# Kernel optimization log

Hardware: AMD Instinct MI355X
Metric: run time of the kernel (lower is better)

Reference implementation:

```python
import jax, jax.numpy as jnp
import numpy as np

N = 100000   # n_nodes (= ninput, identity features)
E = 1600000  # edges per adjacency (avg degree 16)
H = 128      # nhid
EPS = 1e-12


def setup_inputs() -> dict:
    key = jax.random.key(0)
    ks = jax.random.split(key, 24)
    inp = {
        'adj1_rows': jax.random.randint(ks[0], (E,), 0, N),
        'adj1_cols': jax.random.randint(ks[1], (E,), 0, N),
        'adj1_vals': jax.random.uniform(ks[2], (E,), jnp.float32) / 16.0,
        'adj2_rows': jax.random.randint(ks[3], (E,), 0, N),
        'adj2_cols': jax.random.randint(ks[4], (E,), 0, N),
        'adj2_vals': jax.random.uniform(ks[5], (E,), jnp.float32) / 16.0,
    }
    s = 1.0 / np.sqrt(H)
    inp['w1'] = jax.random.uniform(ks[6], (N, H), jnp.float32, -s, s)
    for i in range(2, 10):
        inp[f'w{i}'] = jax.random.uniform(ks[5 + i], (H, H), jnp.float32, -s, s)
    s2 = 1.0 / np.sqrt(2 * H)
    inp['m1'] = jax.random.uniform(ks[15], (H, 2 * H), jnp.float32, -s, s)
    inp['b1'] = jnp.zeros((2 * H,), jnp.float32)
    inp['m2'] = jax.random.uniform(ks[16], (2 * H, 2 * H), jnp.float32, -s2, s2)
    inp['b2'] = jnp.zeros((2 * H,), jnp.float32)
    inp['m3'] = jax.random.uniform(ks[17], (2 * H, 1), jnp.float32, -s2, s2)
    inp['b3'] = jnp.zeros((1,), jnp.float32)
    return inp


def _spmm(rows, cols, vals, x):
    # sparse [N,N] @ dense [N,H] via gather + segment_sum
    return jax.ops.segment_sum(vals[:, None] * x[cols], rows, num_segments=N)


def _l2norm(x):
    # F.normalize(x, p=2, dim=1)
    n = jnp.sqrt(jnp.sum(x * x, axis=1, keepdims=True))
    return x / jnp.maximum(n, EPS)


def _mlp(x, m1, b1, m2, b2, m3, b3):
    # dropout inactive (eval mode) for deterministic reference
    h = jax.nn.relu(x @ m1 + b1)
    h = jax.nn.relu(h @ m2 + b2)
    return h @ m3 + b3  # [N,1]


def _branch(rows, cols, vals, w1, ws, mlp_params):
    x = jax.nn.relu(_spmm(rows, cols, vals, w1))
    x = _l2norm(x)
    score = _mlp(x, *mlp_params)
    for i, w in enumerate(ws):
        x = jax.nn.relu(_spmm(rows, cols, vals, x @ w))
        if i < len(ws) - 1:  # last layer (gc9) is relu only, no normalize
            x = _l2norm(x)
        score = score + _mlp(x, *mlp_params)
    return score


def reference(adj1_rows, adj1_cols, adj1_vals, adj2_rows, adj2_cols, adj2_vals,
              w1, w2, w3, w4, w5, w6, w7, w8, w9,
              m1, b1, m2, b2, m3, b3):
    ws = [w2, w3, w4, w5, w6, w7, w8, w9]
    mlp_params = (m1, b1, m2, b2, m3, b3)
    score1 = _branch(adj1_rows, adj1_cols, adj1_vals, w1, ws, mlp_params)
    score2 = _branch(adj2_rows, adj2_cols, adj2_vals, w1, ws, mlp_params)
    return score1 * score2  # [N,1]
```

## Files before the change

kernel.cpp:

```cpp
#include <hip/hip_runtime.h>
#include <hip/hip_fp16.h>

#define NN 100000
#define NE 1600000
#define HD 128
#define HD2 256

typedef unsigned int u32;
typedef unsigned short u16;
typedef _Float16 half8 __attribute__((ext_vector_type(8)));
typedef float floatx4 __attribute__((ext_vector_type(4)));

static inline int cdiv(int a, int b){ return (a + b - 1) / b; }

__device__ __forceinline__ u32 split_pack(float v){
  __half h;
  if(fabsf(v) < 6.103515625e-05f) h = __ushort_as_half((u16)0);
  else h = __float2half_rn(v);
  float hf = __half2float(h);
  __half l = __float2half_rn((v - hf) * 4096.0f);
  return (u32)__half_as_ushort(h) | ((u32)__half_as_ushort(l) << 16);
}

__global__ void k_zero_int(int* __restrict__ p, int n){
  int i = blockIdx.x * 256 + threadIdx.x;
  if(i < n) p[i] = 0;
}

__global__ void k_zero_f2(float* __restrict__ a, float* __restrict__ b, int n){
  int i = blockIdx.x * 256 + threadIdx.x;
  if(i < n){ a[i] = 0.f; b[i] = 0.f; }
}

__global__ void k_hist(const int* __restrict__ rows, int* __restrict__ cnt){
  int e = blockIdx.x * 256 + threadIdx.x;
  if(e < NE) atomicAdd(&cnt[rows[e]], 1);
}

__global__ void k_scan1(const int* __restrict__ cnt, int* __restrict__ part,
                        int* __restrict__ sums, int n){
  __shared__ int sh[256];
  int tid = threadIdx.x;
  int base = blockIdx.x * 1024 + tid * 4;
  int v0 = (base + 0 < n) ? cnt[base + 0] : 0;
  int v1 = (base + 1 < n) ? cnt[base + 1] : 0;
  int v2 = (base + 2 < n) ? cnt[base + 2] : 0;
  int v3 = (base + 3 < n) ? cnt[base + 3] : 0;
  int s = v0 + v1 + v2 + v3;
  sh[tid] = s;
  __syncthreads();
  for(int d = 1; d < 256; d <<= 1){
    int t = (tid >= d) ? sh[tid - d] : 0;
    __syncthreads();
    sh[tid] += t;
    __syncthreads();
  }
  int excl = sh[tid] - s;
  if(tid == 255) sums[blockIdx.x] = sh[255];
  if(base + 0 < n) part[base + 0] = excl;
  if(base + 1 < n) part[base + 1] = excl + v0;
  if(base + 2 < n) part[base + 2] = excl + v0 + v1;
  if(base + 3 < n) part[base + 3] = excl + v0 + v1 + v2;
}

__global__ void k_scan2(int* __restrict__ sums, int nb){
  __shared__ int sh[128];
  int tid = threadIdx.x;
  int v = (tid < nb) ? sums[tid] : 0;
  sh[tid] = v;
  __syncthreads();
  for(int d = 1; d < 128; d <<= 1){
    int t = (tid >= d) ? sh[tid - d] : 0;
    __syncthreads();
    sh[tid] += t;
    __syncthreads();
  }
  if(tid < nb) sums[tid] = sh[tid] - v;
}

__global__ void k_scan3(int* __restrict__ rowptr, int* __restrict__ cursor,
                        const int* __restrict__ sums, int n){
  int tid = threadIdx.x;
  int off = sums[blockIdx.x];
  int base = blockIdx.x * 1024 + tid * 4;
  #pragma unroll
  for(int j = 0; j < 4; j++){
    int idx = base + j;
    if(idx < n){ int r = rowptr[idx] + off; rowptr[idx] = r; cursor[idx] = r; }
  }
  if(blockIdx.x == 0 && tid == 0) rowptr[n] = NE;
}

__global__ void k_scatter(const int* __restrict__ rows, const int* __restrict__ cols,
                          const float* __restrict__ vals, int* __restrict__ cursor,
                          int* __restrict__ ocol, float* __restrict__ oval){
  int e = blockIdx.x * 256 + threadIdx.x;
  if(e < NE){
    int r = rows[e];
    int pp = atomicAdd(&cursor[r], 1);
    ocol[pp] = cols[e];
    oval[pp] = vals[e];
  }
}

__global__ void k_splitw(const float* __restrict__ W, u32* __restrict__ out,
                         int K, int N, int total){
  int idx = blockIdx.x * 256 + threadIdx.x;
  if(idx < total){
    int n = idx / K, k = idx - n * K;
    out[idx] = split_pack(W[(size_t)k * N + n]);
  }
}

template<bool NORM>
__global__ void k_spmm(const int* __restrict__ rowptr, const int* __restrict__ col,
                       const float* __restrict__ val, const float* __restrict__ X,
                       u32* __restrict__ outpk){
  int node = (blockIdx.x << 2) + (threadIdx.x >> 6);
  int lane = threadIdx.x & 63;
  if(node >= NN) return;
  int s = rowptr[node], e = rowptr[node + 1];
  float ax = 0.f, ay = 0.f, bx = 0.f, by = 0.f;
  float cx = 0.f, cy = 0.f, dx = 0.f, dy = 0.f;
  int i = s;
  for(; i + 7 < e; i += 8){
    int   c0 = col[i],     c1 = col[i + 1], c2 = col[i + 2], c3 = col[i + 3];
    int   c4 = col[i + 4], c5 = col[i + 5], c6 = col[i + 6], c7 = col[i + 7];
    float v0 = val[i],     v1 = val[i + 1], v2 = val[i + 2], v3 = val[i + 3];
    float v4 = val[i + 4], v5 = val[i + 5], v6 = val[i + 6], v7 = val[i + 7];
    float2 x0 = *(const float2*)(X + (size_t)c0 * HD + lane * 2);
    float2 x1 = *(const float2*)(X + (size_t)c1 * HD + lane * 2);
    float2 x2 = *(const float2*)(X + (size_t)c2 * HD + lane * 2);
    float2 x3 = *(const float2*)(X + (size_t)c3 * HD + lane * 2);
    float2 x4 = *(const float2*)(X + (size_t)c4 * HD + lane * 2);
    float2 x5 = *(const float2*)(X + (size_t)c5 * HD + lane * 2);
    float2 x6 = *(const float2*)(X + (size_t)c6 * HD + lane * 2);
    float2 x7 = *(const float2*)(X + (size_t)c7 * HD + lane * 2);
    ax += v0 * x0.x + v1 * x1.x;  ay += v0 * x0.y + v1 * x1.y;
    bx += v2 * x2.x + v3 * x3.x;  by += v2 * x2.y + v3 * x3.y;
    cx += v4 * x4.x + v5 * x5.x;  cy += v4 * x4.y + v5 * x5.y;
    dx += v6 * x6.x + v7 * x7.x;  dy += v6 * x6.y + v7 * x7.y;
  }
  for(; i + 1 < e; i += 2){
    int   c0 = col[i],   c1 = col[i + 1];
    float v0 = val[i],   v1 = val[i + 1];
    float2 x0 = *(const float2*)(X + (size_t)c0 * HD + lane * 2);
    float2 x1 = *(const float2*)(X + (size_t)c1 * HD + lane * 2);
    ax += v0 * x0.x + v1 * x1.x;  ay += v0 * x0.y + v1 * x1.y;
  }
  if(i < e){
    int c = col[i]; float v = val[i];
    float2 xv = *(const float2*)(X + (size_t)c * HD + lane * 2);
    ax += v * xv.x; ay += v * xv.y;
  }
  ax += bx + cx + dx;
  ay += by + cy + dy;
  ax = fmaxf(ax, 0.f);
  ay = fmaxf(ay, 0.f);
  if(NORM){
    float ss = ax * ax + ay * ay;
    #pragma unroll
    for(int o = 32; o >= 1; o >>= 1) ss += __shfl_xor(ss, o, 64);
    float scale = 1.f / fmaxf(sqrtf(ss), 1e-12f);
    ax *= scale; ay *= scale;
  }
  *(uint2*)(outpk + (size_t)node * HD + lane * 2) = make_uint2(split_pack(ax), split_pack(ay));
}

template<int MODE>
__launch_bounds__(256, 2)
__global__ void k_mfma_gemm(const u32* __restrict__ Apk, const u32* __restrict__ Btpk,
                            const float* __restrict__ bias, float* __restrict__ Yout,
                            u32* __restrict__ Hout, const float* __restrict__ m3,
                            float* __restrict__ score, int M, int K, int N){
  __shared__ unsigned short As_h[128 * 40], As_l[128 * 40];
  __shared__ unsigned short Bs_h[128 * 40], Bs_l[128 * 40];
  const int tid = threadIdx.x;
  const int lane = tid & 63, wid = tid >> 6;
  const int lm = lane & 15, lg = lane >> 4;
  const int mq = (wid & 1) * 64, nq = (wid >> 1) * 64;
  const int m0 = blockIdx.x * 128, n0 = blockIdx.y * 128;

  floatx4 accA[4][4], accB[4][4];
  #pragma unroll
  for(int i = 0; i < 4; i++)
    #pragma unroll
    for(int j = 0; j < 4; j++){
      accA[i][j] = (floatx4){0.f, 0.f, 0.f, 0.f};
      accB[i][j] = (floatx4){0.f, 0.f, 0.f, 0.f};
    }

  for(int k0 = 0; k0 < K; k0 += 32){
    uint4 av[4], bv[4];
    #pragma unroll
    for(int j = 0; j < 4; j++){
      int li = tid + j * 256;
      int row = li >> 3, kc = (li & 7) * 4;
      int ar = m0 + row; if(ar >= M) ar = M - 1;
      av[j] = *(const uint4*)(Apk + (size_t)ar * K + k0 + kc);
      bv[j] = *(const uint4*)(Btpk + (size_t)(n0 + row) * K + k0 + kc);
    }
    __syncthreads();
    #pragma unroll
    for(int j = 0; j < 4; j++){
      int li = tid + j * 256;
      int row = li >> 3, kc = (li & 7) * 4;
      int base = row * 40 + kc;
      ushort4 h, l;
      h.x = (u16)(av[j].x & 0xffff); l.x = (u16)(av[j].x >> 16);
      h.y = (u16)(av[j].y & 0xffff); l.y = (u16)(av[j].y >> 16);
      h.z = (u16)(av[j].z & 0xffff); l.z = (u16)(av[j].z >> 16);
      h.w = (u16)(av[j].w & 0xffff); l.w = (u16)(av[j].w >> 16);
      *(ushort4*)&As_h[base] = h;
      *(ushort4*)&As_l[base] = l;
      h.x = (u16)(bv[j].x & 0xffff); l.x = (u16)(bv[j].x >> 16);
      h.y = (u16)(bv[j].y & 0xffff); l.y = (u16)(bv[j].y >> 16);
      h.z = (u16)(bv[j].z & 0xffff); l.z = (u16)(bv[j].z >> 16);
      h.w = (u16)(bv[j].w & 0xffff); l.w = (u16)(bv[j].w >> 16);
      *(ushort4*)&Bs_h[base] = h;
      *(ushort4*)&Bs_l[base] = l;
    }
    __syncthreads();

    half8 fa_h[4], fa_l[4], fb_h[4], fb_l[4];
    #pragma unroll
    for(int s = 0; s < 4; s++){
      int ra = (mq + s * 16 + lm) * 40 + lg * 8;
      fa_h[s] = *(const half8*)&As_h[ra];
      fa_l[s] = *(const half8*)&As_l[ra];
      int rb = (nq + s * 16 + lm) * 40 + lg * 8;
      fb_h[s] = *(const half8*)&Bs_h[rb];
      fb_l[s] = *(const half8*)&Bs_l[rb];
    }
    #pragma unroll
    for(int i = 0; i < 4; i++)
      #pragma unroll
      for(int j = 0; j < 4; j++){
        accA[i][j] = __builtin_amdgcn_mfma_f32_16x16x32_f16(fa_h[i], fb_h[j], accA[i][j], 0, 0, 0);
        accB[i][j] = __builtin_amdgcn_mfma_f32_16x16x32_f16(fa_h[i], fb_l[j], accB[i][j], 0, 0, 0);
        accB[i][j] = __builtin_amdgcn_mfma_f32_16x16x32_f16(fa_l[i], fb_h[j], accB[i][j], 0, 0, 0);
      }
  }

  const float inv4096 = 1.f / 4096.f;
  if(MODE == 0){
    #pragma unroll
    for(int i = 0; i < 4; i++)
      #pragma unroll
      for(int r = 0; r < 4; r++){
        int m = m0 + mq + i * 16 + lg * 4 + r;
        if(m < M){
          #pragma unroll
          for(int j = 0; j < 4; j++){
            int c = n0 + nq + j * 16 + lm;
            Yout[(size_t)m * N + c] = accA[i][j][r] + accB[i][j][r] * inv4096;
          }
        }
      }
  } else if(MODE == 1){
    #pragma unroll
    for(int i = 0; i < 4; i++)
      #pragma unroll
      for(int r = 0; r < 4; r++){
        int m = m0 + mq + i * 16 + lg * 4 + r;
        if(m < M){
          #pragma unroll
          for(int j = 0; j < 4; j++){
            int c = n0 + nq + j * 16 + lm;
            float v = fmaxf(accA[i][j][r] + accB[i][j][r] * inv4096 + bias[c], 0.f);
            Hout[(size_t)m * N + c] = split_pack(v);
          }
        }
      }
  } else {
    #pragma unroll
    for(int i = 0; i < 4; i++)
      #pragma unroll
      for(int r = 0; r < 4; r++){
        float s = 0.f;
        #pragma unroll
        for(int j = 0; j < 4; j++){
          int c = n0 + nq + j * 16 + lm;
          float v = fmaxf(accA[i][j][r] + accB[i][j][r] * inv4096 + bias[c], 0.f);
          s = fmaf(v, m3[c], s);
        }
        s += __shfl_xor(s, 1, 64);
        s += __shfl_xor(s, 2, 64);
        s += __shfl_xor(s, 4, 64);
        s += __shfl_xor(s, 8, 64);
        int m = m0 + mq + i * 16 + lg * 4 + r;
        if(lm == 0 && m < M) atomicAdd(&score[m], s);
      }
  }
}

__global__ void k_final(const float* __restrict__ s1, const float* __restrict__ s2,
                        const float* __restrict__ b3, float* __restrict__ out){
  int i = blockIdx.x * 256 + threadIdx.x;
  if(i < NN){
    float b = 9.f * b3[0];
    out[i] = (s1[i] + b) * (s2[i] + b);
  }
}

extern "C" void kernel_launch(void* const* d_in, const int* in_sizes, int n_in,
                              void* d_out, int out_size, void* d_ws, size_t ws_size,
                              hipStream_t stream){
  const int*   a1r = (const int*)d_in[0];
  const int*   a1c = (const int*)d_in[1];
  const float* a1v = (const float*)d_in[2];
  const int*   a2r = (const int*)d_in[3];
  const int*   a2c = (const int*)d_in[4];
  const float* a2v = (const float*)d_in[5];
  const float* w1  = (const float*)d_in[6];
  const float* w[8];
  for(int i = 0; i < 8; i++) w[i] = (const float*)d_in[7 + i];
  const float* m1 = (const float*)d_in[15];
  const float* b1 = (const float*)d_in[16];
  const float* m2 = (const float*)d_in[17];
  const float* b2 = (const float*)d_in[18];
  const float* m3 = (const float*)d_in[19];
  const float* b3 = (const float*)d_in[20];
  float* out = (float*)d_out;

  char* base = (char*)d_ws;
  size_t off = 0;
  auto alloc = [&](size_t bytes) -> char* {
    char* r = base + off;
    off += (bytes + 255) & ~(size_t)255;
    return r;
  };
  int*   c1ptr = (int*)  alloc((size_t)(NN + 1) * 4);
  int*   c1col = (int*)  alloc((size_t)NE * 4);
  float* c1val = (float*)alloc((size_t)NE * 4);
  int*   c2ptr = (int*)  alloc((size_t)(NN + 1) * 4);
  int*   c2col = (int*)  alloc((size_t)NE * 4);
  float* c2val = (float*)alloc((size_t)NE * 4);
  int*   cursor= (int*)  alloc((size_t)NN * 4);
  int*   sums  = (int*)  alloc(512);
  u32*   xpk   = (u32*)  alloc((size_t)NN * HD * 4);
  u32*   h1pk  = (u32*)  alloc((size_t)NN * HD2 * 4);
  float* sc1   = (float*)alloc((size_t)NN * 4);
  float* sc2   = (float*)alloc((size_t)NN * 4);
  u32*   wtpk[8];
  for(int i = 0; i < 8; i++) wtpk[i] = (u32*)alloc((size_t)HD * HD * 4);
  u32*   m1tpk = (u32*)alloc((size_t)HD2 * HD * 4);
  u32*   m2tpk = (u32*)alloc((size_t)HD2 * HD2 * 4);
  float* y = (float*)h1pk;

  const int SCAN_BLOCKS = cdiv(NN, 1024);
  auto build_csr = [&](const int* rows, const int* cols, const float* vals,
                       int* rptr, int* rcol, float* rval){
    hipLaunchKernelGGL(k_zero_int, dim3(cdiv(NN, 256)), dim3(256), 0, stream, cursor, NN);
    hipLaunchKernelGGL(k_hist,     dim3(cdiv(NE, 256)), dim3(256), 0, stream, rows, cursor);
    hipLaunchKernelGGL(k_scan1,    dim3(SCAN_BLOCKS),   dim3(256), 0, stream, cursor, rptr, sums, NN);
    hipLaunchKernelGGL(k_scan2,    dim3(1),             dim3(128), 0, stream, sums, SCAN_BLOCKS);
    hipLaunchKernelGGL(k_scan3,    dim3(SCAN_BLOCKS),   dim3(256), 0, stream, rptr, cursor, sums, NN);
    hipLaunchKernelGGL(k_scatter,  dim3(cdiv(NE, 256)), dim3(256), 0, stream, rows, cols, vals, cursor, rcol, rval);
  };

  auto splitw = [&](const float* W, u32* o, int K, int N){
    int total = K * N;
    hipLaunchKernelGGL(k_splitw, dim3(cdiv(total, 256)), dim3(256), 0, stream, W, o, K, N, total);
  };
  for(int i = 0; i < 8; i++) splitw(w[i], wtpk[i], HD, HD);
  splitw(m1, m1tpk, HD, HD2);
  splitw(m2, m2tpk, HD2, HD2);

  const int GX = cdiv(NN, 128);
  auto mlp = [&](float* score){
    hipLaunchKernelGGL((k_mfma_gemm<1>), dim3(GX, 2), dim3(256), 0, stream,
                       xpk, m1tpk, b1, (float*)nullptr, h1pk,
                       (const float*)nullptr, (float*)nullptr, NN, HD, HD2);
    hipLaunchKernelGGL((k_mfma_gemm<2>), dim3(GX, 2), dim3(256), 0, stream,
                       h1pk, m2tpk, b2, (float*)nullptr, (u32*)nullptr,
                       m3, score, NN, HD2, HD2);
  };

  auto branch = [&](const int* rptr, const int* rcol, const float* rval, float* score){
    hipLaunchKernelGGL((k_spmm<true>), dim3(cdiv(NN, 4)), dim3(256), 0, stream,
                       rptr, rcol, rval, w1, xpk);
    mlp(score);
    for(int i = 0; i < 8; i++){
      hipLaunchKernelGGL((k_mfma_gemm<0>), dim3(GX, 1), dim3(256), 0, stream,
                         xpk, wtpk[i], (const float*)nullptr, y, (u32*)nullptr,
                         (const float*)nullptr, (float*)nullptr, NN, HD, HD);
      if(i < 7)
        hipLaunchKernelGGL((k_spmm<true>),  dim3(cdiv(NN, 4)), dim3(256), 0, stream,
                           rptr, rcol, rval, y, xpk);
      else
        hipLaunchKernelGGL((k_spmm<false>), dim3(cdiv(NN, 4)), dim3(256), 0, stream,
                           rptr, rcol, rval, y, xpk);
      mlp(score);
    }
  };

  build_csr(a1r, a1c, a1v, c1ptr, c1col, c1val);
  build_csr(a2r, a2c, a2v, c2ptr, c2col, c2val);
  hipLaunchKernelGGL(k_zero_f2, dim3(cdiv(NN, 256)), dim3(256), 0, stream, sc1, sc2, NN);
  branch(c1ptr, c1col, c1val, sc1);
  branch(c2ptr, c2col, c2val, sc2);
  hipLaunchKernelGGL(k_final, dim3(cdiv(NN, 256)), dim3(256), 0, stream, sc1, sc2, b3, out);
}
```

Baseline: 4.860 ms.

## Batch both graph branches into single launches and widen SpMM unroll

Runs the two adjacency branches together: CSR construction, SpMM (via a z grid dimension), and the GEMM/MLP launches now cover 2*N rows when workspace allows, with a fallback to the per-branch path. This halves kernel launch count and gives each GEMM and SpMM launch more blocks to fill the GPU. The SpMM inner loop is also unrolled to 16 gathers in flight. The cost is double-sized intermediate buffers and higher register use in the SpMM kernel.

Result: no change. 4.847 ms (-0.3%).

```diff
diff --git a/kernel.cpp b/kernel.cpp
--- a/kernel.cpp
+++ b/kernel.cpp
@@ -27,25 +27,33 @@
   if(i < n) p[i] = 0;
 }
 
-__global__ void k_zero_f2(float* __restrict__ a, float* __restrict__ b, int n){
+__global__ void k_zero_f(float* __restrict__ p, int n){
   int i = blockIdx.x * 256 + threadIdx.x;
-  if(i < n){ a[i] = 0.f; b[i] = 0.f; }
-}
-
-__global__ void k_hist(const int* __restrict__ rows, int* __restrict__ cnt){
+  if(i < n) p[i] = 0.f;
+}
+
+__global__ void k_hist2(const int* __restrict__ r0, const int* __restrict__ r1,
+                        int* __restrict__ cnt){
   int e = blockIdx.x * 256 + threadIdx.x;
-  if(e < NE) atomicAdd(&cnt[rows[e]], 1);
-}
-
-__global__ void k_scan1(const int* __restrict__ cnt, int* __restrict__ part,
-                        int* __restrict__ sums, int n){
+  if(e < NE){
+    const int* rows = blockIdx.y ? r1 : r0;
+    atomicAdd(&cnt[blockIdx.y * NN + rows[e]], 1);
+  }
+}
+
+__global__ void k_scan1b(const int* __restrict__ cnt, int* __restrict__ p0,
+                         int* __restrict__ p1, int* __restrict__ sums, int n){
   __shared__ int sh[256];
+  int z = blockIdx.y;
+  const int* c = cnt + z * n;
+  int* part = z ? p1 : p0;
+  int* sm = sums + z * 128;
   int tid = threadIdx.x;
   int base = blockIdx.x * 1024 + tid * 4;
-  int v0 = (base + 0 < n) ? cnt[base + 0] : 0;
-  int v1 = (base + 1 < n) ? cnt[base + 1] : 0;
-  int v2 = (base + 2 < n) ? cnt[base + 2] : 0;
-  int v3 = (base + 3 < n) ? cnt[base + 3] : 0;
+  int v0 = (base + 0 < n) ? c[base + 0] : 0;
+  int v1 = (base + 1 < n) ? c[base + 1] : 0;
+  int v2 = (base + 2 < n) ? c[base + 2] : 0;
+  int v3 = (base + 3 < n) ? c[base + 3] : 0;
   int s = v0 + v1 + v2 + v3;
   sh[tid] = s;
   __syncthreads();
@@ -56,17 +64,18 @@
     __syncthreads();
   }
   int excl = sh[tid] - s;
-  if(tid == 255) sums[blockIdx.x] = sh[255];
+  if(tid == 255) sm[blockIdx.x] = sh[255];
   if(base + 0 < n) part[base + 0] = excl;
   if(base + 1 < n) part[base + 1] = excl + v0;
   if(base + 2 < n) part[base + 2] = excl + v0 + v1;
   if(base + 3 < n) part[base + 3] = excl + v0 + v1 + v2;
 }
 
-__global__ void k_scan2(int* __restrict__ sums, int nb){
+__global__ void k_scan2b(int* __restrict__ sums, int nb){
   __shared__ int sh[128];
+  int* s = sums + blockIdx.x * 128;
   int tid = threadIdx.x;
-  int v = (tid < nb) ? sums[tid] : 0;
+  int v = (tid < nb) ? s[tid] : 0;
   sh[tid] = v;
   __syncthreads();
   for(int d = 1; d < 128; d <<= 1){
@@ -75,29 +84,43 @@
     sh[tid] += t;
     __syncthreads();
   }
-  if(tid < nb) sums[tid] = sh[tid] - v;
-}
-
-__global__ void k_scan3(int* __restrict__ rowptr, int* __restrict__ cursor,
-                        const int* __restrict__ sums, int n){
+  if(tid < nb) s[tid] = sh[tid] - v;
+}
+
+__global__ void k_scan3b(int* __restrict__ r0, int* __restrict__ r1,
+                         int* __restrict__ cursor, const int* __restrict__ sums, int n){
+  int z = blockIdx.y;
+  int* rowptr = z ? r1 : r0;
+  int* cur = cursor + z * n;
+  int off = sums[z * 128 + blockIdx.x];
   int tid = threadIdx.x;
-  int off = sums[blockIdx.x];
   int base = blockIdx.x * 1024 + tid * 4;
   #pragma unroll
   for(int j = 0; j < 4; j++){
     int idx = base + j;
-    if(idx < n){ int r = rowptr[idx] + off; rowptr[idx] = r; cursor[idx] = r; }
+    if(idx < n){ int r = rowptr[idx] + off; rowptr[idx] = r; cur[idx] = r; }
   }
   if(blockIdx.x == 0 && tid == 0) rowptr[n] = NE;
 }
 
-__global__ void k_scatter(const int* __restrict__ rows, const int* __restrict__ cols,
-                          const float* __restrict__ vals, int* __restrict__ cursor,
-                          int* __restrict__ ocol, float* __restrict__ oval){
+__global__ void k_scatter2(const int* __restrict__ r0, const int* __restrict__ c0,
+                           const float* __restrict__ v0,
+                           const int* __restrict__ r1, const int* __restrict__ c1,
+                           const float* __restrict__ v1,
+                           int* __restrict__ cursor,
+                           int* __restrict__ oc0, float* __restrict__ ov0,
+                           int* __restrict__ oc1, float* __restrict__ ov1){
   int e = blockIdx.x * 256 + threadIdx.x;
   if(e < NE){
+    int z = blockIdx.y;
+    const int* rows = z ? r1 : r0;
+    const int* cols = z ? c1 : c0;
+    const float* vals = z ? v1 : v0;
+    int* cur = cursor + z * NN;
+    int* ocol = z ? oc1 : oc0;
+    float* oval = z ? ov1 : ov0;
     int r = rows[e];
-    int pp = atomicAdd(&cursor[r], 1);
+    int pp = atomicAdd(&cur[r], 1);
     ocol[pp] = cols[e];
     oval[pp] = vals[e];
   }
@@ -113,9 +136,17 @@
 }
 
 template<bool NORM>
-__global__ void k_spmm(const int* __restrict__ rowptr, const int* __restrict__ col,
-                       const float* __restrict__ val, const float* __restrict__ X,
+__global__ void k_spmm(const int* __restrict__ rp0, const int* __restrict__ col0,
+                       const float* __restrict__ val0,
+                       const int* __restrict__ rp1, const int* __restrict__ col1,
+                       const float* __restrict__ val1,
+                       const float* __restrict__ X0, const float* __restrict__ X1,
                        u32* __restrict__ outpk){
+  int z = blockIdx.z;
+  const int* rowptr = z ? rp1 : rp0;
+  const int* col    = z ? col1 : col0;
+  const float* val  = z ? val1 : val0;
+  const float* X    = z ? X1 : X0;
   int node = (blockIdx.x << 2) + (threadIdx.x >> 6);
   int lane = threadIdx.x & 63;
   if(node >= NN) return;
@@ -123,32 +154,31 @@
   float ax = 0.f, ay = 0.f, bx = 0.f, by = 0.f;
   float cx = 0.f, cy = 0.f, dx = 0.f, dy = 0.f;
   int i = s;
-  for(; i + 7 < e; i += 8){
-    int   c0 = col[i],     c1 = col[i + 1], c2 = col[i + 2], c3 = col[i + 3];
-    int   c4 = col[i + 4], c5 = col[i + 5], c6 = col[i + 6], c7 = col[i + 7];
-    float v0 = val[i],     v1 = val[i + 1], v2 = val[i + 2], v3 = val[i + 3];
-    float v4 = val[i + 4], v5 = val[i + 5], v6 = val[i + 6], v7 = val[i + 7];
-    float2 x0 = *(const float2*)(X + (size_t)c0 * HD + lane * 2);
-    float2 x1 = *(const float2*)(X + (size_t)c1 * HD + lane * 2);
-    float2 x2 = *(const float2*)(X + (size_t)c2 * HD + lane * 2);
-    float2 x3 = *(const float2*)(X + (size_t)c3 * HD + lane * 2);
-    float2 x4 = *(const float2*)(X + (size_t)c4 * HD + lane * 2);
-    float2 x5 = *(const float2*)(X + (size_t)c5 * HD + lane * 2);
-    float2 x6 = *(const float2*)(X + (size_t)c6 * HD + lane * 2);
-    float2 x7 = *(const float2*)(X + (size_t)c7 * HD + lane * 2);
-    ax += v0 * x0.x + v1 * x1.x;  ay += v0 * x0.y + v1 * x1.y;
-    bx += v2 * x2.x + v3 * x3.x;  by += v2 * x2.y + v3 * x3.y;
-    cx += v4 * x4.x + v5 * x5.x;  cy += v4 * x4.y + v5 * x5.y;
-    dx += v6 * x6.x + v7 * x7.x;  dy += v6 * x6.y + v7 * x7.y;
-  }
-  for(; i + 1 < e; i += 2){
-    int   c0 = col[i],   c1 = col[i + 1];
-    float v0 = val[i],   v1 = val[i + 1];
-    float2 x0 = *(const float2*)(X + (size_t)c0 * HD + lane * 2);
-    float2 x1 = *(const float2*)(X + (size_t)c1 * HD + lane * 2);
-    ax += v0 * x0.x + v1 * x1.x;  ay += v0 * x0.y + v1 * x1.y;
-  }
-  if(i < e){
+  for(; i + 15 < e; i += 16){
+    int c[16]; float v[16]; float2 xx[16];
+    #pragma unroll
+    for(int j = 0; j < 16; j++){ c[j] = col[i + j]; v[j] = val[i + j]; }
+    #pragma unroll
+    for(int j = 0; j < 16; j++) xx[j] = *(const float2*)(X + (size_t)c[j] * HD + lane * 2);
+    #pragma unroll
+    for(int j = 0; j < 16; j += 4){
+      ax += v[j] * xx[j].x + v[j+1] * xx[j+1].x;
+      ay += v[j] * xx[j].y + v[j+1] * xx[j+1].y;
+      bx += v[j+2] * xx[j+2].x + v[j+3] * xx[j+3].x;
+      by += v[j+2] * xx[j+2].y + v[j+3] * xx[j+3].y;
+    }
+  }
+  for(; i + 3 < e; i += 4){
+    int   e0 = col[i],   e1 = col[i + 1], e2 = col[i + 2], e3 = col[i + 3];
+    float f0 = val[i],   f1 = val[i + 1], f2 = val[i + 2], f3 = val[i + 3];
+    float2 x0 = *(const float2*)(X + (size_t)e0 * HD + lane * 2);
+    float2 x1 = *(const float2*)(X + (size_t)e1 * HD + lane * 2);
+    float2 x2 = *(const float2*)(X + (size_t)e2 * HD + lane * 2);
+    float2 x3 = *(const float2*)(X + (size_t)e3 * HD + lane * 2);
+    ax += f0 * x0.x + f1 * x1.x;  ay += f0 * x0.y + f1 * x1.y;
+    bx += f2 * x2.x + f3 * x3.x;  by += f2 * x2.y + f3 * x3.y;
+  }
+  for(; i < e; i++){
     int c = col[i]; float v = val[i];
     float2 xv = *(const float2*)(X + (size_t)c * HD + lane * 2);
     ax += v * xv.x; ay += v * xv.y;
@@ -164,7 +194,8 @@
     float scale = 1.f / fmaxf(sqrtf(ss), 1e-12f);
     ax *= scale; ay *= scale;
   }
-  *(uint2*)(outpk + (size_t)node * HD + lane * 2) = make_uint2(split_pack(ax), split_pack(ay));
+  size_t gnode = (size_t)(z * NN + node);
+  *(uint2*)(outpk + gnode * HD + lane * 2) = make_uint2(split_pack(ax), split_pack(ay));
 }
 
 template<int MODE>
@@ -294,12 +325,12 @@
   }
 }
 
-__global__ void k_final(const float* __restrict__ s1, const float* __restrict__ s2,
-                        const float* __restrict__ b3, float* __restrict__ out){
+__global__ void k_final(const float* __restrict__ sc, const float* __restrict__ b3,
+                        float* __restrict__ out){
   int i = blockIdx.x * 256 + threadIdx.x;
   if(i < NN){
     float b = 9.f * b3[0];
-    out[i] = (s1[i] + b) * (s2[i] + b);
+    out[i] = (sc[i] + b) * (sc[NN + i] + b);
   }
 }
 
@@ -336,28 +367,31 @@
   int*   c2ptr = (int*)  alloc((size_t)(NN + 1) * 4);
   int*   c2col = (int*)  alloc((size_t)NE * 4);
   float* c2val = (float*)alloc((size_t)NE * 4);
-  int*   cursor= (int*)  alloc((size_t)NN * 4);
-  int*   sums  = (int*)  alloc(512);
-  u32*   xpk   = (u32*)  alloc((size_t)NN * HD * 4);
-  u32*   h1pk  = (u32*)  alloc((size_t)NN * HD2 * 4);
-  float* sc1   = (float*)alloc((size_t)NN * 4);
-  float* sc2   = (float*)alloc((size_t)NN * 4);
+  int*   cursor= (int*)  alloc((size_t)2 * NN * 4);
+  int*   sums  = (int*)  alloc(1024);
+  float* sc    = (float*)alloc((size_t)2 * NN * 4);
   u32*   wtpk[8];
   for(int i = 0; i < 8; i++) wtpk[i] = (u32*)alloc((size_t)HD * HD * 4);
   u32*   m1tpk = (u32*)alloc((size_t)HD2 * HD * 4);
   u32*   m2tpk = (u32*)alloc((size_t)HD2 * HD2 * 4);
+
+  size_t fixed = off;
+  size_t need_batched = fixed + (((size_t)2*NN*HD*4 + 255) & ~(size_t)255)
+                              + (((size_t)2*NN*HD2*4 + 255) & ~(size_t)255);
+  bool batched = (ws_size >= need_batched);
+  int MB = batched ? 2 * NN : NN;
+  u32*   xpk  = (u32*)alloc((size_t)MB * HD * 4);
+  u32*   h1pk = (u32*)alloc((size_t)MB * HD2 * 4);
   float* y = (float*)h1pk;
 
+  hipLaunchKernelGGL(k_zero_int, dim3(cdiv(2 * NN, 256)), dim3(256), 0, stream, cursor, 2 * NN);
+  hipLaunchKernelGGL(k_hist2, dim3(cdiv(NE, 256), 2), dim3(256), 0, stream, a1r, a2r, cursor);
   const int SCAN_BLOCKS = cdiv(NN, 1024);
-  auto build_csr = [&](const int* rows, const int* cols, const float* vals,
-                       int* rptr, int* rcol, float* rval){
-    hipLaunchKernelGGL(k_zero_int, dim3(cdiv(NN, 256)), dim3(256), 0, stream, cursor, NN);
-    hipLaunchKernelGGL(k_hist,     dim3(cdiv(NE, 256)), dim3(256), 0, stream, rows, cursor);
-    hipLaunchKernelGGL(k_scan1,    dim3(SCAN_BLOCKS),   dim3(256), 0, stream, cursor, rptr, sums, NN);
-    hipLaunchKernelGGL(k_scan2,    dim3(1),             dim3(128), 0, stream, sums, SCAN_BLOCKS);
-    hipLaunchKernelGGL(k_scan3,    dim3(SCAN_BLOCKS),   dim3(256), 0, stream, rptr, cursor, sums, NN);
-    hipLaunchKernelGGL(k_scatter,  dim3(cdiv(NE, 256)), dim3(256), 0, stream, rows, cols, vals, cursor, rcol, rval);
-  };
+  hipLaunchKernelGGL(k_scan1b, dim3(SCAN_BLOCKS, 2), dim3(256), 0, stream, cursor, c1ptr, c2ptr, sums, NN);
+  hipLaunchKernelGGL(k_scan2b, dim3(2), dim3(128), 0, stream, sums, SCAN_BLOCKS);
+  hipLaunchKernelGGL(k_scan3b, dim3(SCAN_BLOCKS, 2), dim3(256), 0, stream, c1ptr, c2ptr, cursor, sums, NN);
+  hipLaunchKernelGGL(k_scatter2, dim3(cdiv(NE, 256), 2), dim3(256), 0, stream,
+                     a1r, a1c, a1v, a2r, a2c, a2v, cursor, c1col, c1val, c2col, c2val);
 
   auto splitw = [&](const float* W, u32* o, int K, int N){
     int total = K * N;
@@ -367,38 +401,59 @@
   splitw(m1, m1tpk, HD, HD2);
   splitw(m2, m2tpk, HD2, HD2);
 
-  const int GX = cdiv(NN, 128);
-  auto mlp = [&](float* score){
-    hipLaunchKernelGGL((k_mfma_gemm<1>), dim3(GX, 2), dim3(256), 0, stream,
+  hipLaunchKernelGGL(k_zero_f, dim3(cdiv(2 * NN, 256)), dim3(256), 0, stream, sc, 2 * NN);
+
+  auto mlp = [&](int M, float* score){
+    int gx = cdiv(M, 128);
+    hipLaunchKernelGGL((k_mfma_gemm<1>), dim3(gx, 2), dim3(256), 0, stream,
                        xpk, m1tpk, b1, (float*)nullptr, h1pk,
-                       (const float*)nullptr, (float*)nullptr, NN, HD, HD2);
-    hipLaunchKernelGGL((k_mfma_gemm<2>), dim3(GX, 2), dim3(256), 0, stream,
+                       (const float*)nullptr, (float*)nullptr, M, HD, HD2);
+    hipLaunchKernelGGL((k_mfma_gemm<2>), dim3(gx, 2), dim3(256), 0, stream,
                        h1pk, m2tpk, b2, (float*)nullptr, (u32*)nullptr,
-                       m3, score, NN, HD2, HD2);
+                       m3, score, M, HD2, HD2);
   };
 
-  auto branch = [&](const int* rptr, const int* rcol, const float* rval, float* score){
-    hipLaunchKernelGGL((k_spmm<true>), dim3(cdiv(NN, 4)), dim3(256), 0, stream,
-                       rptr, rcol, rval, w1, xpk);
-    mlp(score);
+  if(batched){
+    hipLaunchKernelGGL((k_spmm<true>), dim3(cdiv(NN, 4), 1, 2), dim3(256), 0, stream,
+                       c1ptr, c1col, c1val, c2ptr, c2col, c2val, w1, w1, xpk);
+    mlp(2 * NN, sc);
     for(int i = 0; i < 8; i++){
-      hipLaunchKernelGGL((k_mfma_gemm<0>), dim3(GX, 1), dim3(256), 0, stream,
+      hipLaunchKernelGGL((k_mfma_gemm<0>), dim3(cdiv(2 * NN, 128), 1), dim3(256), 0, stream,
                          xpk, wtpk[i], (const float*)nullptr, y, (u32*)nullptr,
-                         (const float*)nullptr, (float*)nullptr, NN, HD, HD);
+                         (const float*)nullptr, (float*)nullptr, 2 * NN, HD, HD);
       if(i < 7)
-        hipLaunchKernelGGL((k_spmm<true>),  dim3(cdiv(NN, 4)), dim3(256), 0, stream,
-                           rptr, rcol, rval, y, xpk);
+        hipLaunchKernelGGL((k_spmm<true>), dim3(cdiv(NN, 4), 1, 2), dim3(256), 0, stream,
+                           c1ptr, c1col, c1val, c2ptr, c2col, c2val,
+                           y, y + (size_t)NN * HD, xpk);
       else
-        hipLaunchKernelGGL((k_spmm<false>), dim3(cdiv(NN, 4)), dim3(256), 0, stream,
-                           rptr, rcol, rval, y, xpk);
-      mlp(score);
-    }
-  };
-
-  build_csr(a1r, a1c, a1v, c1ptr, c1col, c1val);
-  build_csr(a2r, a2c, a2v, c2ptr, c2col, c2val);
-  hipLaunchKernelGGL(k_zero_f2, dim3(cdiv(NN, 256)), dim3(256), 0, stream, sc1, sc2, NN);
-  branch(c1ptr, c1col, c1val, sc1);
-  branch(c2ptr, c2col, c2val, sc2);
-  hipLaunchKernelGGL(k_final, dim3(cdiv(NN, 256)), dim3(256), 0, stream, sc1, sc2, b3, out);
-}
+        hipLaunchKernelGGL((k_spmm<false>), dim3(cdiv(NN, 4), 1, 2), dim3(256), 0, stream,
+                           c1ptr, c1col, c1val, c2ptr, c2col, c2val,
+                           y, y + (size_t)NN * HD, xpk);
+      mlp(2 * NN, sc);
+    }
+  } else {
+    for(int b = 0; b < 2; b++){
+      const int* rp = b ? c2ptr : c1ptr;
+      const int* cc = b ? c2col : c1col;
+      const float* vv = b ? c2val : c1val;
+      float* score = sc + (size_t)b * NN;
+      hipLaunchKernelGGL((k_spmm<true>), dim3(cdiv(NN, 4), 1, 1), dim3(256), 0, stream,
+                         rp, cc, vv, rp, cc, vv, w1, w1, xpk);
+      mlp(NN, score);
+      for(int i = 0; i < 8; i++){
+        hipLaunchKernelGGL((k_mfma_gemm<0>), dim3(cdiv(NN, 128), 1), dim3(256), 0, stream,
+                           xpk, wtpk[i], (const float*)nullptr, y, (u32*)nullptr,
+                           (const float*)nullptr, (float*)nullptr, NN, HD, HD);
+        if(i < 7)
+          hipLaunchKernelGGL((k_spmm<true>), dim3(cdiv(NN, 4), 1, 1), dim3(256), 0, stream,
+                             rp, cc, vv, rp, cc, vv, y, y, xpk);
+        else
+          hipLaunchKernelGGL((k_spmm<false>), dim3(cdiv(NN, 4), 1, 1), dim3(256), 0, stream,
+                             rp, cc, vv, rp, cc, vv, y, y, xpk);
+        mlp(NN, score);
+      }
+    }
+  }
+
+  hipLaunchKernelGGL(k_final, dim3(cdiv(NN, 256)), dim3(256), 0, stream, sc, b3, out);
+}
```

## Co-schedule MLP second GEMM with next SpMM via work-queue fused kernel

Applied to the files above, without the earlier changes.

Packs CSR column and value into one interleaved uint2 array and unrolls the SpMM gather loop to 16 edges. Adds a persistent fused kernel in which blocks pull work from atomic queues, so the MLP's second GEMM for one layer runs alongside the following layer's SpMM. This needs a separate y buffer so the two do not conflict, and falls back to the old path when the workspace is too small. The CSR is now built per branch and reuses one buffer. The aim is to overlap the compute-bound GEMM with the memory-bound gather and to cut index loads; the risks are queue overhead, load imbalance, and a fixed grid of 1024 blocks.

Result: slower. 6.410 ms (+31.9%).

```diff
diff --git a/kernel.cpp b/kernel.cpp
--- a/kernel.cpp
+++ b/kernel.cpp
@@ -27,9 +27,9 @@
   if(i < n) p[i] = 0;
 }
 
-__global__ void k_zero_f2(float* __restrict__ a, float* __restrict__ b, int n){
+__global__ void k_zero_f(float* __restrict__ p, int n){
   int i = blockIdx.x * 256 + threadIdx.x;
-  if(i < n){ a[i] = 0.f; b[i] = 0.f; }
+  if(i < n) p[i] = 0.f;
 }
 
 __global__ void k_hist(const int* __restrict__ rows, int* __restrict__ cnt){
@@ -93,13 +93,12 @@
 
 __global__ void k_scatter(const int* __restrict__ rows, const int* __restrict__ cols,
                           const float* __restrict__ vals, int* __restrict__ cursor,
-                          int* __restrict__ ocol, float* __restrict__ oval){
+                          uint2* __restrict__ ecv){
   int e = blockIdx.x * 256 + threadIdx.x;
   if(e < NE){
     int r = rows[e];
     int pp = atomicAdd(&cursor[r], 1);
-    ocol[pp] = cols[e];
-    oval[pp] = vals[e];
+    ecv[pp] = make_uint2((u32)cols[e], __float_as_uint(vals[e]));
   }
 }
 
@@ -112,59 +111,65 @@
   }
 }
 
+__device__ __forceinline__ void spmm_node(int node, int lane,
+                                          const int* __restrict__ rowptr,
+                                          const uint2* __restrict__ ecv,
+                                          const float* __restrict__ X,
+                                          u32* __restrict__ outpk, int norm){
+  int s = rowptr[node], e = rowptr[node + 1];
+  float ax = 0.f, ay = 0.f, bx = 0.f, by = 0.f;
+  int i = s;
+  for(; i + 15 < e; i += 16){
+    uint2 ee[16]; float2 xx[16];
+    #pragma unroll
+    for(int j = 0; j < 16; j++) ee[j] = ecv[i + j];
+    #pragma unroll
+    for(int j = 0; j < 16; j++) xx[j] = *(const float2*)(X + (size_t)ee[j].x * HD + lane * 2);
+    #pragma unroll
+    for(int j = 0; j < 16; j += 4){
+      ax += __uint_as_float(ee[j].y)   * xx[j].x   + __uint_as_float(ee[j+1].y) * xx[j+1].x;
+      ay += __uint_as_float(ee[j].y)   * xx[j].y   + __uint_as_float(ee[j+1].y) * xx[j+1].y;
+      bx += __uint_as_float(ee[j+2].y) * xx[j+2].x + __uint_as_float(ee[j+3].y) * xx[j+3].x;
+      by += __uint_as_float(ee[j+2].y) * xx[j+2].y + __uint_as_float(ee[j+3].y) * xx[j+3].y;
+    }
+  }
+  for(; i + 3 < e; i += 4){
+    uint2 e0 = ecv[i], e1 = ecv[i+1], e2 = ecv[i+2], e3 = ecv[i+3];
+    float2 x0 = *(const float2*)(X + (size_t)e0.x * HD + lane * 2);
+    float2 x1 = *(const float2*)(X + (size_t)e1.x * HD + lane * 2);
+    float2 x2 = *(const float2*)(X + (size_t)e2.x * HD + lane * 2);
+    float2 x3 = *(const float2*)(X + (size_t)e3.x * HD + lane * 2);
+    ax += __uint_as_float(e0.y) * x0.x + __uint_as_float(e1.y) * x1.x;
+    ay += __uint_as_float(e0.y) * x0.y + __uint_as_float(e1.y) * x1.y;
+    bx += __uint_as_float(e2.y) * x2.x + __uint_as_float(e3.y) * x3.x;
+    by += __uint_as_float(e2.y) * x2.y + __uint_as_float(e3.y) * x3.y;
+  }
+  for(; i < e; i++){
+    uint2 e0 = ecv[i];
+    float2 xv = *(const float2*)(X + (size_t)e0.x * HD + lane * 2);
+    ax += __uint_as_float(e0.y) * xv.x;
+    ay += __uint_as_float(e0.y) * xv.y;
+  }
+  ax += bx; ay += by;
+  ax = fmaxf(ax, 0.f);
+  ay = fmaxf(ay, 0.f);
+  if(norm){
+    float ss = ax * ax + ay * ay;
+    #pragma unroll
+    for(int o = 32; o >= 1; o >>= 1) ss += __shfl_xor(ss, o, 64);
+    float scale = 1.f / fmaxf(sqrtf(ss), 1e-12f);
+    ax *= scale; ay *= scale;
+  }
+  *(uint2*)(outpk + (size_t)node * HD + lane * 2) = make_uint2(split_pack(ax), split_pack(ay));
+}
+
 template<bool NORM>
-__global__ void k_spmm(const int* __restrict__ rowptr, const int* __restrict__ col,
-                       const float* __restrict__ val, const float* __restrict__ X,
-                       u32* __restrict__ outpk){
+__global__ void k_spmm(const int* __restrict__ rowptr, const uint2* __restrict__ ecv,
+                       const float* __restrict__ X, u32* __restrict__ outpk){
   int node = (blockIdx.x << 2) + (threadIdx.x >> 6);
   int lane = threadIdx.x & 63;
   if(node >= NN) return;
-  int s = rowptr[node], e = rowptr[node + 1];
-  float ax = 0.f, ay = 0.f, bx = 0.f, by = 0.f;
-  float cx = 0.f, cy = 0.f, dx = 0.f, dy = 0.f;
-  int i = s;
-  for(; i + 7 < e; i += 8){
-    int   c0 = col[i],     c1 = col[i + 1], c2 = col[i + 2], c3 = col[i + 3];
-    int   c4 = col[i + 4], c5 = col[i + 5], c6 = col[i + 6], c7 = col[i + 7];
-    float v0 = val[i],     v1 = val[i + 1], v2 = val[i + 2], v3 = val[i + 3];
-    float v4 = val[i + 4], v5 = val[i + 5], v6 = val[i + 6], v7 = val[i + 7];
-    float2 x0 = *(const float2*)(X + (size_t)c0 * HD + lane * 2);
-    float2 x1 = *(const float2*)(X + (size_t)c1 * HD + lane * 2);
-    float2 x2 = *(const float2*)(X + (size_t)c2 * HD + lane * 2);
-    float2 x3 = *(const float2*)(X + (size_t)c3 * HD + lane * 2);
-    float2 x4 = *(const float2*)(X + (size_t)c4 * HD + lane * 2);
-    float2 x5 = *(const float2*)(X + (size_t)c5 * HD + lane * 2);
-    float2 x6 = *(const float2*)(X + (size_t)c6 * HD + lane * 2);
-    float2 x7 = *(const float2*)(X + (size_t)c7 * HD + lane * 2);
-    ax += v0 * x0.x + v1 * x1.x;  ay += v0 * x0.y + v1 * x1.y;
-    bx += v2 * x2.x + v3 * x3.x;  by += v2 * x2.y + v3 * x3.y;
-    cx += v4 * x4.x + v5 * x5.x;  cy += v4 * x4.y + v5 * x5.y;
-    dx += v6 * x6.x + v7 * x7.x;  dy += v6 * x6.y + v7 * x7.y;
-  }
-  for(; i + 1 < e; i += 2){
-    int   c0 = col[i],   c1 = col[i + 1];
-    float v0 = val[i],   v1 = val[i + 1];
-    float2 x0 = *(const float2*)(X + (size_t)c0 * HD + lane * 2);
-    float2 x1 = *(const float2*)(X + (size_t)c1 * HD + lane * 2);
-    ax += v0 * x0.x + v1 * x1.x;  ay += v0 * x0.y + v1 * x1.y;
-  }
-  if(i < e){
-    int c = col[i]; float v = val[i];
-    float2 xv = *(const float2*)(X + (size_t)c * HD + lane * 2);
-    ax += v * xv.x; ay += v * xv.y;
-  }
-  ax += bx + cx + dx;
-  ay += by + cy + dy;
-  ax = fmaxf(ax, 0.f);
-  ay = fmaxf(ay, 0.f);
-  if(NORM){
-    float ss = ax * ax + ay * ay;
-    #pragma unroll
-    for(int o = 32; o >= 1; o >>= 1) ss += __shfl_xor(ss, o, 64);
-    float scale = 1.f / fmaxf(sqrtf(ss), 1e-12f);
-    ax *= scale; ay *= scale;
-  }
-  *(uint2*)(outpk + (size_t)node * HD + lane * 2) = make_uint2(split_pack(ax), split_pack(ay));
+  spmm_node(node, lane, rowptr, ecv, X, outpk, NORM ? 1 : 0);
 }
 
 template<int MODE>
@@ -173,8 +178,8 @@
                             const float* __restrict__ bias, float* __restrict__ Yout,
                             u32* __restrict__ Hout, const float* __restrict__ m3,
                             float* __restrict__ score, int M, int K, int N){
-  __shared__ unsigned short As_h[128 * 40], As_l[128 * 40];
-  __shared__ unsigned short Bs_h[128 * 40], Bs_l[128 * 40];
+  __shared__ u16 As_h[128 * 40], As_l[128 * 40];
+  __shared__ u16 Bs_h[128 * 40], Bs_l[128 * 40];
   const int tid = threadIdx.x;
   const int lane = tid & 63, wid = tid >> 6;
   const int lm = lane & 15, lg = lane >> 4;
@@ -294,12 +299,135 @@
   }
 }
 
-__global__ void k_final(const float* __restrict__ s1, const float* __restrict__ s2,
-                        const float* __restrict__ b3, float* __restrict__ out){
+__launch_bounds__(256, 2)
+__global__ void k_fused(const u32* __restrict__ Apk, const u32* __restrict__ Btpk,
+                        const float* __restrict__ bias, const float* __restrict__ m3,
+                        float* __restrict__ score, int M, int Ngi,
+                        const int* __restrict__ rowptr, const uint2* __restrict__ ecv,
+                        const float* __restrict__ X, u32* __restrict__ outpk,
+                        int norm, int* __restrict__ qa, int* __restrict__ qb){
+  __shared__ u16 As_h[128 * 40], As_l[128 * 40];
+  __shared__ u16 Bs_h[128 * 40], Bs_l[128 * 40];
+  __shared__ int s_item;
+  const int tid = threadIdx.x;
+  const int lane = tid & 63, wid = tid >> 6;
+  const int lm = lane & 15, lg = lane >> 4;
+  const int mq = (wid & 1) * 64, nq = (wid >> 1) * 64;
+  const int K = HD2;
+  const float inv4096 = 1.f / 4096.f;
+
+  auto do_gemm = [&](int g){
+    int m0 = (g >> 1) * 128, n0 = (g & 1) * 128;
+    floatx4 accA[4][4], accB[4][4];
+    #pragma unroll
+    for(int i = 0; i < 4; i++)
+      #pragma unroll
+      for(int j = 0; j < 4; j++){
+        accA[i][j] = (floatx4){0.f, 0.f, 0.f, 0.f};
+        accB[i][j] = (floatx4){0.f, 0.f, 0.f, 0.f};
+      }
+    for(int k0 = 0; k0 < K; k0 += 32){
+      uint4 av[4], bv[4];
+      #pragma unroll
+      for(int j = 0; j < 4; j++){
+        int li = tid + j * 256;
+        int row = li >> 3, kc = (li & 7) * 4;
+        int ar = m0 + row; if(ar >= M) ar = M - 1;
+        av[j] = *(const uint4*)(Apk + (size_t)ar * K + k0 + kc);
+        bv[j] = *(const uint4*)(Btpk + (size_t)(n0 + row) * K + k0 + kc);
+      }
+      __syncthreads();
+      #pragma unroll
+      for(int j = 0; j < 4; j++){
+        int li = tid + j * 256;
+        int row = li >> 3, kc = (li & 7) * 4;
+        int base = row * 40 + kc;
+        ushort4 h, l;
+        h.x = (u16)(av[j].x & 0xffff); l.x = (u16)(av[j].x >> 16);
+        h.y = (u16)(av[j].y & 0xffff); l.y = (u16)(av[j].y >> 16);
+        h.z = (u16)(av[j].z & 0xffff); l.z = (u16)(av[j].z >> 16);
+        h.w = (u16)(av[j].w & 0xffff); l.w = (u16)(av[j].w >> 16);
+        *(ushort4*)&As_h[base] = h;
+        *(ushort4*)&As_l[base] = l;
+        h.x = (u16)(bv[j].x & 0xffff); l.x = (u16)(bv[j].x >> 16);
+        h.y = (u16)(bv[j].y & 0xffff); l.y = (u16)(bv[j].y >> 16);
+        h.z = (u16)(bv[j].z & 0xffff); l.z = (u16)(bv[j].z >> 16);
+        h.w = (u16)(bv[j].w & 0xffff); l.w = (u16)(bv[j].w >> 16);
+        *(ushort4*)&Bs_h[base] = h;
+        *(ushort4*)&Bs_l[base] = l;
+      }
+      __syncthreads();
+      half8 fa_h[4], fa_l[4], fb_h[4], fb_l[4];
+      #pragma unroll
+      for(int s = 0; s < 4; s++){
+        int ra = (mq + s * 16 + lm) * 40 + lg * 8;
+        fa_h[s] = *(const half8*)&As_h[ra];
+        fa_l[s] = *(const half8*)&As_l[ra];
+        int rb = (nq + s * 16 + lm) * 40 + lg * 8;
+        fb_h[s] = *(const half8*)&Bs_h[rb];
+        fb_l[s] = *(const half8*)&Bs_l[rb];
+      }
+      #pragma unroll
+      for(int i = 0; i < 4; i++)
+        #pragma unroll
+        for(int j = 0; j < 4; j++){
+          accA[i][j] = __builtin_amdgcn_mfma_f32_16x16x32_f16(fa_h[i], fb_h[j], accA[i][j], 0, 0, 0);
+          accB[i][j] = __builtin_amdgcn_mfma_f32_16x16x32_f16(fa_h[i], fb_l[j], accB[i][j], 0, 0, 0);
+          accB[i][j] = __builtin_amdgcn_mfma_f32_16x16x32_f16(fa_l[i], fb_h[j], accB[i][j], 0, 0, 0);
+        }
+    }
+    #pragma unroll
+    for(int i = 0; i < 4; i++)
+      #pragma unroll
+      for(int r = 0; r < 4; r++){
+        float s = 0.f;
+        #pragma unroll
+        for(int j = 0; j < 4; j++){
+          int c = n0 + nq + j * 16 + lm;
+          float v = fmaxf(accA[i][j][r] + accB[i][j][r] * inv4096 + bias[c], 0.f);
+          s = fmaf(v, m3[c], s);
+        }
+        s += __shfl_xor(s, 1, 64);
+        s += __shfl_xor(s, 2, 64);
+        s += __shfl_xor(s, 4, 64);
+        s += __shfl_xor(s, 8, 64);
+        int m = m0 + mq + i * 16 + lg * 4 + r;
+        if(lm == 0 && m < M) atomicAdd(&score[m], s);
+      }
+  };
+
+  auto gemm_loop = [&](){
+    for(;;){
+      __syncthreads();
+      if(tid == 0) s_item = atomicAdd(qa, 1);
+      __syncthreads();
+      int g = s_item;
+      if(g >= Ngi) break;
+      do_gemm(g);
+    }
+  };
+  auto spmm_loop = [&](){
+    for(;;){
+      int s;
+      if(lane == 0) s = atomicAdd(qb, 16);
+      s = __shfl(s, 0, 64);
+      if(s >= NN) break;
+      int e = s + 16; if(e > NN) e = NN;
+      for(int n = s; n < e; n++)
+        spmm_node(n, lane, rowptr, ecv, X, outpk, norm);
+    }
+  };
+
+  if((blockIdx.x & 1) == 0){ gemm_loop(); spmm_loop(); }
+  else                     { spmm_loop(); __syncthreads(); gemm_loop(); }
+}
+
+__global__ void k_final(const float* __restrict__ sc, const float* __restrict__ b3,
+                        float* __restrict__ out){
   int i = blockIdx.x * 256 + threadIdx.x;
   if(i < NN){
     float b = 9.f * b3[0];
-    out[i] = (s1[i] + b) * (s2[i] + b);
+    out[i] = (sc[i] + b) * (sc[NN + i] + b);
   }
 }
 
@@ -330,33 +458,30 @@
     off += (bytes + 255) & ~(size_t)255;
     return r;
   };
-  int*   c1ptr = (int*)  alloc((size_t)(NN + 1) * 4);
-  int*   c1col = (int*)  alloc((size_t)NE * 4);
-  float* c1val = (float*)alloc((size_t)NE * 4);
-  int*   c2ptr = (int*)  alloc((size_t)(NN + 1) * 4);
-  int*   c2col = (int*)  alloc((size_t)NE * 4);
-  float* c2val = (float*)alloc((size_t)NE * 4);
+  int*   cptr  = (int*)  alloc((size_t)(NN + 1) * 4);
+  uint2* ecv   = (uint2*)alloc((size_t)NE * 8);
   int*   cursor= (int*)  alloc((size_t)NN * 4);
   int*   sums  = (int*)  alloc(512);
-  u32*   xpk   = (u32*)  alloc((size_t)NN * HD * 4);
-  u32*   h1pk  = (u32*)  alloc((size_t)NN * HD2 * 4);
-  float* sc1   = (float*)alloc((size_t)NN * 4);
-  float* sc2   = (float*)alloc((size_t)NN * 4);
+  float* sc    = (float*)alloc((size_t)2 * NN * 4);
+  int*   qcnt  = (int*)  alloc(64 * 4);
   u32*   wtpk[8];
   for(int i = 0; i < 8; i++) wtpk[i] = (u32*)alloc((size_t)HD * HD * 4);
   u32*   m1tpk = (u32*)alloc((size_t)HD2 * HD * 4);
   u32*   m2tpk = (u32*)alloc((size_t)HD2 * HD2 * 4);
-  float* y = (float*)h1pk;
+  u32*   xpk   = (u32*)alloc((size_t)NN * HD * 4);
+  u32*   h1pk  = (u32*)alloc((size_t)NN * HD2 * 4);
+  size_t need_fused = off + (((size_t)NN * HD * 4 + 255) & ~(size_t)255);
+  bool fused_tier = (ws_size >= need_fused);
+  float* y = fused_tier ? (float*)alloc((size_t)NN * HD * 4) : (float*)h1pk;
 
   const int SCAN_BLOCKS = cdiv(NN, 1024);
-  auto build_csr = [&](const int* rows, const int* cols, const float* vals,
-                       int* rptr, int* rcol, float* rval){
+  auto build_csr = [&](const int* rows, const int* cols, const float* vals){
     hipLaunchKernelGGL(k_zero_int, dim3(cdiv(NN, 256)), dim3(256), 0, stream, cursor, NN);
     hipLaunchKernelGGL(k_hist,     dim3(cdiv(NE, 256)), dim3(256), 0, stream, rows, cursor);
-    hipLaunchKernelGGL(k_scan1,    dim3(SCAN_BLOCKS),   dim3(256), 0, stream, cursor, rptr, sums, NN);
+    hipLaunchKernelGGL(k_scan1,    dim3(SCAN_BLOCKS),   dim3(256), 0, stream, cursor, cptr, sums, NN);
     hipLaunchKernelGGL(k_scan2,    dim3(1),             dim3(128), 0, stream, sums, SCAN_BLOCKS);
-    hipLaunchKernelGGL(k_scan3,    dim3(SCAN_BLOCKS),   dim3(256), 0, stream, rptr, cursor, sums, NN);
-    hipLaunchKernelGGL(k_scatter,  dim3(cdiv(NE, 256)), dim3(256), 0, stream, rows, cols, vals, cursor, rcol, rval);
+    hipLaunchKernelGGL(k_scan3,    dim3(SCAN_BLOCKS),   dim3(256), 0, stream, cptr, cursor, sums, NN);
+    hipLaunchKernelGGL(k_scatter,  dim3(cdiv(NE, 256)), dim3(256), 0, stream, rows, cols, vals, cursor, ecv);
   };
 
   auto splitw = [&](const float* W, u32* o, int K, int N){
@@ -366,39 +491,60 @@
   for(int i = 0; i < 8; i++) splitw(w[i], wtpk[i], HD, HD);
   splitw(m1, m1tpk, HD, HD2);
   splitw(m2, m2tpk, HD2, HD2);
+  hipLaunchKernelGGL(k_zero_f, dim3(cdiv(2 * NN, 256)), dim3(256), 0, stream, sc, 2 * NN);
+  hipLaunchKernelGGL(k_zero_int, dim3(1), dim3(256), 0, stream, qcnt, 64);
 
   const int GX = cdiv(NN, 128);
-  auto mlp = [&](float* score){
+  const int Ngi = GX * 2;
+  auto mode1 = [&](){
     hipLaunchKernelGGL((k_mfma_gemm<1>), dim3(GX, 2), dim3(256), 0, stream,
                        xpk, m1tpk, b1, (float*)nullptr, h1pk,
                        (const float*)nullptr, (float*)nullptr, NN, HD, HD2);
+  };
+  auto mode2 = [&](float* score){
     hipLaunchKernelGGL((k_mfma_gemm<2>), dim3(GX, 2), dim3(256), 0, stream,
                        h1pk, m2tpk, b2, (float*)nullptr, (u32*)nullptr,
                        m3, score, NN, HD2, HD2);
   };
-
-  auto branch = [&](const int* rptr, const int* rcol, const float* rval, float* score){
+  auto gemm0 = [&](int i){
+    hipLaunchKernelGGL((k_mfma_gemm<0>), dim3(GX, 1), dim3(256), 0, stream,
+                       xpk, wtpk[i], (const float*)nullptr, y, (u32*)nullptr,
+                       (const float*)nullptr, (float*)nullptr, NN, HD, HD);
+  };
+
+  for(int b = 0; b < 2; b++){
+    if(b == 0) build_csr(a1r, a1c, a1v);
+    else       build_csr(a2r, a2c, a2v);
+    float* score = sc + (size_t)b * NN;
     hipLaunchKernelGGL((k_spmm<true>), dim3(cdiv(NN, 4)), dim3(256), 0, stream,
-                       rptr, rcol, rval, w1, xpk);
-    mlp(score);
-    for(int i = 0; i < 8; i++){
-      hipLaunchKernelGGL((k_mfma_gemm<0>), dim3(GX, 1), dim3(256), 0, stream,
-                         xpk, wtpk[i], (const float*)nullptr, y, (u32*)nullptr,
-                         (const float*)nullptr, (float*)nullptr, NN, HD, HD);
-      if(i < 7)
-        hipLaunchKernelGGL((k_spmm<true>),  dim3(cdiv(NN, 4)), dim3(256), 0, stream,
-                           rptr, rcol, rval, y, xpk);
-      else
-        hipLaunchKernelGGL((k_spmm<false>), dim3(cdiv(NN, 4)), dim3(256), 0, stream,
-                           rptr, rcol, rval, y, xpk);
-      mlp(score);
-    }
-  };
-
-  build_csr(a1r, a1c, a1v, c1ptr, c1col, c1val);
-  build_csr(a2r, a2c, a2v, c2ptr, c2col, c2val);
-  hipLaunchKernelGGL(k_zero_f2, dim3(cdiv(NN, 256)), dim3(256), 0, stream, sc1, sc2, NN);
-  branch(c1ptr, c1col, c1val, sc1);
-  branch(c2ptr, c2col, c2val, sc2);
-  hipLaunchKernelGGL(k_final, dim3(cdiv(NN, 256)), dim3(256), 0, stream, sc1, sc2, b3, out);
-}
+                       cptr, ecv, w1, xpk);
+    if(fused_tier){
+      for(int i = 0; i < 8; i++){
+        mode1();
+        gemm0(i);
+        int* qa = qcnt + (b * 8 + i) * 2;
+        hipLaunchKernelGGL(k_fused, dim3(1024), dim3(256), 0, stream,
+                           h1pk, m2tpk, b2, m3, score, NN, Ngi,
+                           cptr, ecv, y, xpk, (i < 7) ? 1 : 0, qa, qa + 1);
+      }
+      mode1();
+      mode2(score);
+    } else {
+      mode1();
+      mode2(score);
+      for(int i = 0; i < 8; i++){
+        gemm0(i);
+        if(i < 7)
+          hipLaunchKernelGGL((k_spmm<true>),  dim3(cdiv(NN, 4)), dim3(256), 0, stream,
+                             cptr, ecv, y, xpk);
+        else
+          hipLaunchKernelGGL((k_spmm<false>), dim3(cdiv(NN, 4)), dim3(256), 0, stream,
+                             cptr, ecv, y, xpk);
+        mode1();
+        mode2(score);
+      }
+    }
+  }
+
+  hipLaunchKernelGGL(k_final, dim3(cdiv(NN, 256)), dim3(256), 0, stream, sc, b3, out);
+}
```
